# Kernel tuning notes

Hardware: AMD Instinct MI355X
Metric: run time of the kernel (lower is better)

The kernel has to match this reference:

```python
import jax, jax.numpy as jnp
import numpy as np


def _gru(x, w_ih, w_hh, b_ih, b_hh):
    # x: [B, T, D]; torch nn.GRU (batch_first) semantics, h0 = 0
    B = x.shape[0]
    H = w_hh.shape[1]
    def step(h, xt):
        gi = xt @ w_ih.T + b_ih          # [B, 3H]
        gh = h @ w_hh.T + b_hh           # [B, 3H]
        ir, iz, inn = jnp.split(gi, 3, axis=-1)
        hr, hz, hn = jnp.split(gh, 3, axis=-1)
        r = jax.nn.sigmoid(ir + hr)
        z = jax.nn.sigmoid(iz + hz)
        n = jnp.tanh(inn + r * hn)
        h_new = (1.0 - z) * n + z * h
        return h_new, h_new
    h0 = jnp.zeros((B, H), x.dtype)
    _, ys = jax.lax.scan(step, h0, jnp.swapaxes(x, 0, 1))
    return jnp.swapaxes(ys, 0, 1)        # [B, T, H]


def setup_inputs() -> dict:
    key = jax.random.key(0)
    ks = iter(jax.random.split(key, 40))
    def p(shape, scale=0.05):
        return jax.random.normal(next(ks), shape, dtype=jnp.float32) * scale
    B, T, Z, S = 1024, 2, 100, 6
    return {
        "x": p((B, T, Z, S), 1.0),
        # actor: GRU(6 -> 64) + SimpleSubActor(64 -> 512 -> 128 -> 1)
        "a_gru_wih": p((192, 6)), "a_gru_whh": p((192, 64)),
        "a_gru_bih": p((192,)), "a_gru_bhh": p((192,)),
        "a_fc1_w": p((512, 64)), "a_fc1_b": p((512,)),
        "a_fc2_w": p((128, 512)), "a_fc2_b": p((128,)),
        "a_fc3_w": p((1, 128)), "a_fc3_b": p((1,)),
        # critic: GRU(35 -> 32) + SimpleSubCritic(32 -> 512 -> 256 -> 1)
        "c_gru_wih": p((96, 35)), "c_gru_whh": p((96, 32)),
        "c_gru_bih": p((96,)), "c_gru_bhh": p((96,)),
        "c_fc1_w": p((512, 32)), "c_fc1_b": p((512,)),
        "c_fc2_w": p((256, 512)), "c_fc2_b": p((256,)),
        "c_fc3_w": p((1, 256)), "c_fc3_b": p((1,)),
        # LocalizedModule(35 -> 512 -> 256 -> 1)
        "lm_fc1_w": p((512, 35)), "lm_fc1_b": p((512,)),
        "lm_fc2_w": p((256, 512)), "lm_fc2_b": p((256,)),
        "lm_fc3_w": p((1, 256)), "lm_fc3_b": p((1,)),
    }


def reference(x, a_gru_wih, a_gru_whh, a_gru_bih, a_gru_bhh,
              a_fc1_w, a_fc1_b, a_fc2_w, a_fc2_b, a_fc3_w, a_fc3_b,
              c_gru_wih, c_gru_whh, c_gru_bih, c_gru_bhh,
              c_fc1_w, c_fc1_b, c_fc2_w, c_fc2_b, c_fc3_w, c_fc3_b,
              lm_fc1_w, lm_fc1_b, lm_fc2_w, lm_fc2_b, lm_fc3_w, lm_fc3_b):
    B, T, Z, S = x.shape
    # ---- SimpleActor: same GRU+MLP shared across zones -> batch zones ----
    # torch: a[i] from x[:, :, i]; torch.stack(a) -> [Z, B, T, 1], then .view(-1, T, Z)
    xz = jnp.transpose(x, (2, 0, 1, 3)).reshape(Z * B, T, S)   # zones-major
    sx = _gru(xz, a_gru_wih, a_gru_whh, a_gru_bih, a_gru_bhh)  # [Z*B, T, 64]
    h = jax.nn.relu(sx @ a_fc1_w.T + a_fc1_b)
    h = jax.nn.relu(h @ a_fc2_w.T + a_fc2_b)
    sa = h @ a_fc3_w.T + a_fc3_b                               # [Z*B, T, 1]
    p = sa.reshape(-1, T, Z)                                   # faithful view(-1, t, nzones)
    # ---- concat action onto state ----
    xc = jnp.concatenate([x, p.reshape(-1, T, Z, 1)], axis=-1)  # [B, T, Z, 7]
    # ---- SimpleCritic: f/q lists reset each iter -> only zone i=99 survives ----
    # neighbors of 99: (99, 89, 100->zeros, 109->zeros, 98)
    zeros = jnp.zeros_like(xc[:, :, Z - 1])
    xi = jnp.concatenate([xc[:, :, 99], xc[:, :, 89], zeros, zeros, xc[:, :, 98]], axis=2)  # [B, T, 35]
    # LocalizedModule on last timestep
    hf = jax.nn.relu(xi[:, -1, :] @ lm_fc1_w.T + lm_fc1_b)
    hf = jax.nn.relu(hf @ lm_fc2_w.T + lm_fc2_b)
    f = hf @ lm_fc3_w.T + lm_fc3_b                             # [B, 1]
    # critic GRU + SimpleSubCritic (it keeps only last timestep)
    xq = _gru(xi, c_gru_wih, c_gru_whh, c_gru_bih, c_gru_bhh)  # [B, T, 32]
    hq = jax.nn.relu(xq[:, -1, :] @ c_fc1_w.T + c_fc1_b)
    hq = jax.nn.relu(hq @ c_fc2_w.T + c_fc2_b)
    qz = hq @ c_fc3_w.T + c_fc3_b                              # [B, 1]
    q = jnp.sum(f + qz, axis=1)                                # [B]
    return p[:, -1], q.reshape(-1, 1)
```

## Files before the change

kernel.cpp:

```cpp
#include <hip/hip_runtime.h>
#include <hip/hip_bf16.h>

#define NB 1024
#define NT 2
#define NZ 100
#define NS 6
#define NSEQ (NZ*NB)

typedef short short8 __attribute__((ext_vector_type(8)));
typedef float floatx4 __attribute__((ext_vector_type(4)));
typedef unsigned int uint2v __attribute__((ext_vector_type(2)));

__device__ __forceinline__ float sigm(float v)     { return 1.0f/(1.0f + __expf(-v)); }
__device__ __forceinline__ float tanhfast(float v) { float t = __expf(2.0f*v); return 1.0f - 2.0f/(t + 1.0f); }
__device__ __forceinline__ unsigned short f2bf(float f) {
    __hip_bfloat16 h = __float2bfloat16(f);
    return *reinterpret_cast<unsigned short*>(&h);
}

#define WS_WIHB   819200
#define WS_WHHB   (WS_WIHB + 192*32*2)
#define WS_W1B    (WS_WHHB + 192*64*2)
#define WS_W2B    (WS_W1B + 512*64*2)
#define WS_L1WB   (WS_W2B + 128*512*2)
#define WS_L2WB   (WS_L1WB + 512*64*2)
#define WS_CF1WB  (WS_L2WB + 256*512*2)
#define WS_CF2WB  (WS_CF1WB + 512*32*2)
#define WS_CWIHB  (WS_CF2WB + 256*512*2)
#define WS_CWHHB  (WS_CWIHB + 96*64*2)

#define PREP_N (116736 + 32768 + 131072 + 16384 + 131072 + 6144 + 3072)

__global__ __launch_bounds__(256)
void prep_kernel(const float* __restrict__ wih, const float* __restrict__ whh,
                 const float* __restrict__ w1,  const float* __restrict__ w2,
                 const float* __restrict__ l1w, const float* __restrict__ l2w,
                 const float* __restrict__ cf1w, const float* __restrict__ cf2w,
                 const float* __restrict__ cwih, const float* __restrict__ cwhh,
                 unsigned short* wihb, unsigned short* whhb,
                 unsigned short* w1b,  unsigned short* w2b,
                 unsigned short* l1wb, unsigned short* l2wb,
                 unsigned short* cf1wb, unsigned short* cf2wb,
                 unsigned short* cwihb, unsigned short* cwhhb)
{
    int e = blockIdx.x*256 + threadIdx.x;
    if (e < 6144) {
        int g = e >> 5, k = e & 31;
        wihb[e] = f2bf(k < 6 ? wih[g*6 + k] : 0.0f);
    } else if (e < 18432) {
        int i = e - 6144;  whhb[i] = f2bf(whh[i]);
    } else if (e < 51200) {
        int i = e - 18432; w1b[i] = f2bf(w1[i]);
    } else if (e < 116736) {
        int i = e - 51200; w2b[i] = f2bf(w2[i]);
    } else if (e < 149504) {
        int i = e - 116736; int o = i >> 6, k = i & 63;
        l1wb[i] = f2bf(k < 35 ? l1w[o*35 + k] : 0.0f);
    } else if (e < 280576) {
        int i = e - 149504; l2wb[i] = f2bf(l2w[i]);
    } else if (e < 296960) {
        int i = e - 280576; cf1wb[i] = f2bf(cf1w[i]);
    } else if (e < 428032) {
        int i = e - 296960; cf2wb[i] = f2bf(cf2w[i]);
    } else if (e < 434176) {
        int i = e - 428032; int o = i >> 6, k = i & 63;
        cwihb[i] = f2bf(k < 35 ? cwih[o*35 + k] : 0.0f);
    } else if (e < PREP_N) {
        int i = e - 434176; cwhhb[i] = f2bf(cwhh[i]);
    }
}

__device__ __forceinline__ int swz(int r) { return (r & 7) << 4; }

__device__ __forceinline__ short8 ldsfrag(const char* base, int rowstride, int r, int k0) {
    int byte = r*rowstride + k0*2;
    byte ^= swz(r);
    return *reinterpret_cast<const short8*>(base + byte);
}

__device__ __forceinline__ short8 xfrag(const float* __restrict__ xp) {
    float2 a  = *reinterpret_cast<const float2*>(xp);
    float2 b2 = *reinterpret_cast<const float2*>(xp + 2);
    float2 c  = *reinterpret_cast<const float2*>(xp + 4);
    short8 f;
    f[0] = (short)f2bf(a.x);  f[1] = (short)f2bf(a.y);
    f[2] = (short)f2bf(b2.x); f[3] = (short)f2bf(b2.y);
    f[4] = (short)f2bf(c.x);  f[5] = (short)f2bf(c.y);
    f[6] = 0; f[7] = 0;
    return f;
}

__global__ __launch_bounds__(256)
void actor_mfma(const float* __restrict__ x,
                const unsigned short* __restrict__ wihb, const unsigned short* __restrict__ whhb,
                const float* __restrict__ bih, const float* __restrict__ bhh,
                const unsigned short* __restrict__ w1b, const float* __restrict__ b1,
                const unsigned short* __restrict__ w2b, const float* __restrict__ b2,
                const float* __restrict__ w3, const float* __restrict__ b3,
                float* __restrict__ sa, float* __restrict__ out0)
{
    __shared__ __align__(16) char smem[40960];
    char*  sxb  = smem;
    float* fc3p = (float*)smem;
    char*  h1b  = smem + 8192;

    const int tid  = threadIdx.x;
    const int wv   = tid >> 6;
    const int lane = tid & 63;
    const int r16  = lane & 15;
    const int g4   = lane >> 4;
    const int ft   = wv;
    const int s0   = blockIdx.x * 32;
    const int zz   = s0 >> 10;
    const int b0   = s0 & 1023;

    const int fb = ft*16 + g4*4;
    const floatx4 bihR = *reinterpret_cast<const floatx4*>(bih + fb);
    const floatx4 bihZ = *reinterpret_cast<const floatx4*>(bih + 64 + fb);
    const floatx4 bihN = *reinterpret_cast<const floatx4*>(bih + 128 + fb);
    const floatx4 bhhR = *reinterpret_cast<const floatx4*>(bhh + fb);
    const floatx4 bhhZ = *reinterpret_cast<const floatx4*>(bhh + 64 + fb);
    const floatx4 bhhN = *reinterpret_cast<const floatx4*>(bhh + 128 + fb);

    floatx4 h0v[2];
    floatx4 g1R[2], g1Z[2], g1N[2];

    {
        const short8 aR = *reinterpret_cast<const short8*>(wihb + ((ft     )*16 + r16)*32 + g4*8);
        const short8 aZ = *reinterpret_cast<const short8*>(wihb + ((ft +  4)*16 + r16)*32 + g4*8);
        const short8 aN = *reinterpret_cast<const short8*>(wihb + ((ft +  8)*16 + r16)*32 + g4*8);
        #pragma unroll
        for (int u = 0; u < 2; ++u) {
            const int seq = u*16 + r16;
            const float* xrow = x + (((b0 + seq)*NT)*NZ + zz)*NS;
            short8 bx0 = xfrag(xrow);
            short8 bx1 = xfrag(xrow + NZ*NS);
            floatx4 gR = {0,0,0,0}, gZ = {0,0,0,0}, gN = {0,0,0,0};
            gR = __builtin_amdgcn_mfma_f32_16x16x32_bf16(aR, bx0, gR, 0, 0, 0);
            gZ = __builtin_amdgcn_mfma_f32_16x16x32_bf16(aZ, bx0, gZ, 0, 0, 0);
            gN = __builtin_amdgcn_mfma_f32_16x16x32_bf16(aN, bx0, gN, 0, 0, 0);
            floatx4 tR = {0,0,0,0}, tZ = {0,0,0,0}, tN = {0,0,0,0};
            tR = __builtin_amdgcn_mfma_f32_16x16x32_bf16(aR, bx1, tR, 0, 0, 0);
            tZ = __builtin_amdgcn_mfma_f32_16x16x32_bf16(aZ, bx1, tZ, 0, 0, 0);
            tN = __builtin_amdgcn_mfma_f32_16x16x32_bf16(aN, bx1, tN, 0, 0, 0);
            g1R[u] = tR; g1Z[u] = tZ; g1N[u] = tN;
            floatx4 hh;
            #pragma unroll
            for (int q = 0; q < 4; ++q) {
                float r = sigm(gR[q] + bihR[q] + bhhR[q]);
                float z = sigm(gZ[q] + bihZ[q] + bhhZ[q]);
                float n = tanhfast(gN[q] + bihN[q] + r*bhhN[q]);
                hh[q] = (1.0f - z)*n;
            }
            h0v[u] = hh;
            unsigned int lo = (unsigned int)f2bf(hh[0]) | ((unsigned int)f2bf(hh[1]) << 16);
            unsigned int hi = (unsigned int)f2bf(hh[2]) | ((unsigned int)f2bf(hh[3]) << 16);
            uint2v vv = {lo, hi};
            int ba = seq*128 + fb*2; ba ^= swz(seq);
            *reinterpret_cast<uint2v*>(sxb + ba) = vv;
        }
    }
    __syncthreads();

    {
        const short8 wR0 = *reinterpret_cast<const short8*>(whhb + ((ft     )*16 + r16)*64 + g4*8);
        const short8 wR1 = *reinterpret_cast<const short8*>(whhb + ((ft     )*16 + r16)*64 + 32 + g4*8);
        const short8 wZ0 = *reinterpret_cast<const short8*>(whhb + ((ft +  4)*16 + r16)*64 + g4*8);
        const short8 wZ1 = *reinterpret_cast<const short8*>(whhb + ((ft +  4)*16 + r16)*64 + 32 + g4*8);
        const short8 wN0 = *reinterpret_cast<const short8*>(whhb + ((ft +  8)*16 + r16)*64 + g4*8);
        const short8 wN1 = *reinterpret_cast<const short8*>(whhb + ((ft +  8)*16 + r16)*64 + 32 + g4*8);
        #pragma unroll
        for (int u = 0; u < 2; ++u) {
            const int seq = u*16 + r16;
            short8 bh0 = ldsfrag(sxb, 128, seq, g4*8);
            short8 bh1 = ldsfrag(sxb, 128, seq, 32 + g4*8);
            floatx4 hR = {0,0,0,0}, hZ = {0,0,0,0}, hN = {0,0,0,0};
            hR = __builtin_amdgcn_mfma_f32_16x16x32_bf16(wR0, bh0, hR, 0, 0, 0);
            hZ = __builtin_amdgcn_mfma_f32_16x16x32_bf16(wZ0, bh0, hZ, 0, 0, 0);
            hN = __builtin_amdgcn_mfma_f32_16x16x32_bf16(wN0, bh0, hN, 0, 0, 0);
            hR = __builtin_amdgcn_mfma_f32_16x16x32_bf16(wR1, bh1, hR, 0, 0, 0);
            hZ = __builtin_amdgcn_mfma_f32_16x16x32_bf16(wZ1, bh1, hZ, 0, 0, 0);
            hN = __builtin_amdgcn_mfma_f32_16x16x32_bf16(wN1, bh1, hN, 0, 0, 0);
            floatx4 hn;
            #pragma unroll
            for (int q = 0; q < 4; ++q) {
                float r = sigm(g1R[u][q] + bihR[q] + hR[q] + bhhR[q]);
                float z = sigm(g1Z[u][q] + bihZ[q] + hZ[q] + bhhZ[q]);
                float n = tanhfast(g1N[u][q] + bihN[q] + r*(hN[q] + bhhN[q]));
                hn[q] = (1.0f - z)*n + z*h0v[u][q];
            }
            unsigned int lo = (unsigned int)f2bf(hn[0]) | ((unsigned int)f2bf(hn[1]) << 16);
            unsigned int hi = (unsigned int)f2bf(hn[2]) | ((unsigned int)f2bf(hn[3]) << 16);
            uint2v vv = {lo, hi};
            int row = 32 + seq;
            int ba = row*128 + fb*2; ba ^= swz(row);
            *reinterpret_cast<uint2v*>(sxb + ba) = vv;
        }
    }
    __syncthreads();

    short8 fr[4][2];
    #pragma unroll
    for (int rt = 0; rt < 4; ++rt) {
        fr[rt][0] = ldsfrag(sxb, 128, rt*16 + r16, g4*8);
        fr[rt][1] = ldsfrag(sxb, 128, rt*16 + r16, 32 + g4*8);
    }

    const int mt0 = wv*2, mt1 = wv*2 + 1;
    floatx4 acc[2][4];
    {
        const floatx4 bA = *reinterpret_cast<const floatx4*>(b2 + mt0*16 + g4*4);
        const floatx4 bB = *reinterpret_cast<const floatx4*>(b2 + mt1*16 + g4*4);
        #pragma unroll
        for (int rt = 0; rt < 4; ++rt) { acc[0][rt] = bA; acc[1][rt] = bB; }
    }

    #pragma unroll
    for (int h = 0; h < 2; ++h) {
        #pragma unroll
        for (int j = 0; j < 4; ++j) {
            int mtg = h*16 + wv*4 + j;
            int mtl = wv*4 + j;
            const short8 a0 = *reinterpret_cast<const short8*>(w1b + (mtg*16 + r16)*64 + g4*8);
            const short8 a1 = *reinterpret_cast<const short8*>(w1b + (mtg*16 + r16)*64 + 32 + g4*8);
            const floatx4 bias = *reinterpret_cast<const floatx4*>(b1 + mtg*16 + g4*4);
            #pragma unroll
            for (int rt = 0; rt < 4; ++rt) {
                floatx4 a = bias;
                a = __builtin_amdgcn_mfma_f32_16x16x32_bf16(a0, fr[rt][0], a, 0, 0, 0);
                a = __builtin_amdgcn_mfma_f32_16x16x32_bf16(a1, fr[rt][1], a, 0, 0, 0);
                unsigned int lo = (unsigned int)f2bf(fmaxf(a[0],0.f)) | ((unsigned int)f2bf(fmaxf(a[1],0.f)) << 16);
                unsigned int hi = (unsigned int)f2bf(fmaxf(a[2],0.f)) | ((unsigned int)f2bf(fmaxf(a[3],0.f)) << 16);
                int row = rt*16 + r16;
                int byte = row*512 + (mtl*16 + g4*4)*2; byte ^= swz(row);
                uint2v vv = {lo, hi};
                *reinterpret_cast<uint2v*>(h1b + byte) = vv;
            }
        }
        __syncthreads();

        {
            const unsigned short* wp0 = w2b + (mt0*16 + r16)*512 + h*256 + g4*8;
            const unsigned short* wp1 = w2b + (mt1*16 + r16)*512 + h*256 + g4*8;
            #pragma unroll
            for (int ks = 0; ks < 8; ++ks) {
                const short8 a0 = *reinterpret_cast<const short8*>(wp0 + ks*32);
                const short8 a1 = *reinterpret_cast<const short8*>(wp1 + ks*32);
                #pragma unroll
                for (int rt = 0; rt < 4; ++rt) {
                    short8 bb = ldsfrag(h1b, 512, rt*16 + r16, ks*32 + g4*8);
                    acc[0][rt] = __builtin_amdgcn_mfma_f32_16x16x32_bf16(a0, bb, acc[0][rt], 0, 0, 0);
                    acc[1][rt] = __builtin_amdgcn_mfma_f32_16x16x32_bf16(a1, bb, acc[1][rt], 0, 0, 0);
                }
            }
        }
        if (h == 0) __syncthreads();
    }

    {
        const floatx4 w3a = *reinterpret_cast<const floatx4*>(w3 + mt0*16 + g4*4);
        const floatx4 w3b = *reinterpret_cast<const floatx4*>(w3 + mt1*16 + g4*4);
        #pragma unroll
        for (int rt = 0; rt < 4; ++rt) {
            float p = fmaxf(acc[0][rt][0],0.f)*w3a[0] + fmaxf(acc[0][rt][1],0.f)*w3a[1]
                    + fmaxf(acc[0][rt][2],0.f)*w3a[2] + fmaxf(acc[0][rt][3],0.f)*w3a[3]
                    + fmaxf(acc[1][rt][0],0.f)*w3b[0] + fmaxf(acc[1][rt][1],0.f)*w3b[1]
                    + fmaxf(acc[1][rt][2],0.f)*w3b[2] + fmaxf(acc[1][rt][3],0.f)*w3b[3];
            p += __shfl_xor(p, 16);
            p += __shfl_xor(p, 32);
            if (g4 == 0) fc3p[wv*64 + rt*16 + r16] = p;
        }
    }
    __syncthreads();

    if (tid < 64) {
        float v = b3[0];
        #pragma unroll
        for (int w = 0; w < 4; ++w) v += fc3p[w*64 + tid];
        int t = tid >> 5, sl = tid & 31;
        int gseq = s0 + sl;
        int i = gseq*2 + t;
        sa[i] = v;
        int m = i % 200;
        if (m >= 100) out0[(i/200)*NZ + (m - 100)] = v;
    }
}

__global__ __launch_bounds__(512)
void critic_mfma(const float* __restrict__ x, const float* __restrict__ sa,
                 const unsigned short* __restrict__ cwihb, const unsigned short* __restrict__ cwhhb,
                 const float* __restrict__ cbih, const float* __restrict__ cbhh,
                 const unsigned short* __restrict__ cf1wb, const float* __restrict__ cf1b,
                 const unsigned short* __restrict__ cf2wb, const float* __restrict__ cf2b,
                 const float* __restrict__ cf3w, const float* __restrict__ cf3b,
                 const unsigned short* __restrict__ l1wb, const float* __restrict__ l1b,
                 const unsigned short* __restrict__ l2wb, const float* __restrict__ l2b,
                 const float* __restrict__ l3w, const float* __restrict__ l3b,
                 float* __restrict__ outq)
{
    __shared__ __align__(16) char smem[25600];
    char*  xib = smem;
    char*  h1b = smem + 4096;
    char*  h0b = smem + 20480;
    char*  hqb = smem + 22528;
    float* fp  = (float*)(smem + 24576);
    float* qp  = (float*)(smem + 25088);

    const int tid  = threadIdx.x;
    const int wv   = tid >> 6;
    const int lane = tid & 63;
    const int r16  = lane & 15;
    const int g4   = lane >> 4;
    const int b0   = blockIdx.x * 16;

    for (int e = tid; e < 2048; e += 512) {
        int trow = e >> 6, k = e & 63;
        int t = trow >> 4, row = trow & 15;
        int b = b0 + row;
        float v = 0.0f;
        if (k < 35) {
            int slot = k / 7, s = k - slot*7;
            int nb = (slot==0)?99:((slot==1)?89:((slot==4)?98:-1));
            if (nb >= 0) v = (s < 6) ? x[((b*NT + t)*NZ + nb)*NS + s]
                                     : sa[b*200 + t*100 + nb];
        }
        int byte = trow*128 + k*2; byte ^= ((trow & 7) << 4);
        *reinterpret_cast<unsigned short*>(xib + byte) = f2bf(v);
    }
    __syncthreads();

    {
        short8 bx0 = ldsfrag(xib, 128, 16 + r16, g4*8);
        short8 bx1 = ldsfrag(xib, 128, 16 + r16, 32 + g4*8);
        #pragma unroll
        for (int j = 0; j < 4; ++j) {
            int mt = wv*4 + j;
            const short8 a0 = *reinterpret_cast<const short8*>(l1wb + (mt*16 + r16)*64 + g4*8);
            const short8 a1 = *reinterpret_cast<const short8*>(l1wb + (mt*16 + r16)*64 + 32 + g4*8);
            floatx4 acc = *reinterpret_cast<const floatx4*>(l1b + mt*16 + g4*4);
            acc = __builtin_amdgcn_mfma_f32_16x16x32_bf16(a0, bx0, acc, 0, 0, 0);
            acc = __builtin_amdgcn_mfma_f32_16x16x32_bf16(a1, bx1, acc, 0, 0, 0);
            unsigned int lo = (unsigned int)f2bf(fmaxf(acc[0],0.f)) | ((unsigned int)f2bf(fmaxf(acc[1],0.f)) << 16);
            unsigned int hi = (unsigned int)f2bf(fmaxf(acc[2],0.f)) | ((unsigned int)f2bf(fmaxf(acc[3],0.f)) << 16);
            int byte = r16*1024 + (mt*16 + g4*4)*2; byte ^= ((r16 & 7) << 4);
            uint2v vv = {lo, hi};
            *reinterpret_cast<uint2v*>(h1b + byte) = vv;
        }
    }
    __syncthreads();

    {
        int mt0 = wv*2, mt1 = wv*2 + 1;
        floatx4 acc0 = *reinterpret_cast<const floatx4*>(l2b + mt0*16 + g4*4);
        floatx4 acc1 = *reinterpret_cast<const floatx4*>(l2b + mt1*16 + g4*4);
        const unsigned short* wp0 = l2wb + (mt0*16 + r16)*512 + g4*8;
        const unsigned short* wp1 = l2wb + (mt1*16 + r16)*512 + g4*8;
        for (int ks = 0; ks < 16; ++ks) {
            short8 bb = ldsfrag(h1b, 1024, r16, ks*32 + g4*8);
            const short8 a0 = *reinterpret_cast<const short8*>(wp0 + ks*32);
            const short8 a1 = *reinterpret_cast<const short8*>(wp1 + ks*32);
            acc0 = __builtin_amdgcn_mfma_f32_16x16x32_bf16(a0, bb, acc0, 0, 0, 0);
            acc1 = __builtin_amdgcn_mfma_f32_16x16x32_bf16(a1, bb, acc1, 0, 0, 0);
        }
        const floatx4 w0 = *reinterpret_cast<const floatx4*>(l3w + mt0*16 + g4*4);
        const floatx4 w1 = *reinterpret_cast<const floatx4*>(l3w + mt1*16 + g4*4);
        float p = fmaxf(acc0[0],0.f)*w0[0] + fmaxf(acc0[1],0.f)*w0[1]
                + fmaxf(acc0[2],0.f)*w0[2] + fmaxf(acc0[3],0.f)*w0[3]
                + fmaxf(acc1[0],0.f)*w1[0] + fmaxf(acc1[1],0.f)*w1[1]
                + fmaxf(acc1[2],0.f)*w1[2] + fmaxf(acc1[3],0.f)*w1[3];
        p += __shfl_xor(p, 16);
        p += __shfl_xor(p, 32);
        if (g4 == 0) fp[wv*16 + r16] = p;
    }
    __syncthreads();

    floatx4 h0r = {0,0,0,0};
    floatx4 gR1 = {0,0,0,0}, gZ1 = {0,0,0,0}, gN1 = {0,0,0,0};
    floatx4 bihR, bihZ, bihN, bhhR, bhhZ, bhhN;
    if (wv < 2) {
        const int hf = wv;
        const int fb = hf*16 + g4*4;
        bihR = *reinterpret_cast<const floatx4*>(cbih + fb);
        bihZ = *reinterpret_cast<const floatx4*>(cbih + 32 + fb);
        bihN = *reinterpret_cast<const floatx4*>(cbih + 64 + fb);
        bhhR = *reinterpret_cast<const floatx4*>(cbhh + fb);
        bhhZ = *reinterpret_cast<const floatx4*>(cbhh + 32 + fb);
        bhhN = *reinterpret_cast<const floatx4*>(cbhh + 64 + fb);
        short8 bx0 = ldsfrag(xib, 128, r16, g4*8);
        short8 bx1 = ldsfrag(xib, 128, r16, 32 + g4*8);
        short8 cx0 = ldsfrag(xib, 128, 16 + r16, g4*8);
        short8 cx1 = ldsfrag(xib, 128, 16 + r16, 32 + g4*8);
        floatx4 gR0 = {0,0,0,0}, gZ0 = {0,0,0,0}, gN0 = {0,0,0,0};
        #pragma unroll
        for (int p = 0; p < 2; ++p) {
            const short8 aR = *reinterpret_cast<const short8*>(cwihb + ((hf    )*16 + r16)*64 + p*32 + g4*8);
            const short8 aZ = *reinterpret_cast<const short8*>(cwihb + ((2+hf  )*16 + r16)*64 + p*32 + g4*8);
            const short8 aN = *reinterpret_cast<const short8*>(cwihb + ((4+hf  )*16 + r16)*64 + p*32 + g4*8);
            short8 b0f = p ? bx1 : bx0;
            short8 b1f = p ? cx1 : cx0;
            gR0 = __builtin_amdgcn_mfma_f32_16x16x32_bf16(aR, b0f, gR0, 0, 0, 0);
            gZ0 = __builtin_amdgcn_mfma_f32_16x16x32_bf16(aZ, b0f, gZ0, 0, 0, 0);
            gN0 = __builtin_amdgcn_mfma_f32_16x16x32_bf16(aN, b0f, gN0, 0, 0, 0);
            gR1 = __builtin_amdgcn_mfma_f32_16x16x32_bf16(aR, b1f, gR1, 0, 0, 0);
            gZ1 = __builtin_amdgcn_mfma_f32_16x16x32_bf16(aZ, b1f, gZ1, 0, 0, 0);
            gN1 = __builtin_amdgcn_mfma_f32_16x16x32_bf16(aN, b1f, gN1, 0, 0, 0);
        }
        #pragma unroll
        for (int q = 0; q < 4; ++q) {
            float r = sigm(gR0[q] + bihR[q] + bhhR[q]);
            float z = sigm(gZ0[q] + bihZ[q] + bhhZ[q]);
            float n = tanhfast(gN0[q] + bihN[q] + r*bhhN[q]);
            h0r[q] = (1.0f - z)*n;
        }
        unsigned int lo = (unsigned int)f2bf(h0r[0]) | ((unsigned int)f2bf(h0r[1]) << 16);
        unsigned int hi = (unsigned int)f2bf(h0r[2]) | ((unsigned int)f2bf(h0r[3]) << 16);
        uint2v vv = {lo, hi};
        int byte = r16*128 + fb*2; byte ^= ((r16 & 7) << 4);
        *reinterpret_cast<uint2v*>(h0b + byte) = vv;
    }
    __syncthreads();
    if (wv < 2) {
        const int hf = wv;
        const int fb = hf*16 + g4*4;
        short8 bh = ldsfrag(h0b, 128, r16, g4*8);
        const short8 aR = *reinterpret_cast<const short8*>(cwhhb + ((hf    )*16 + r16)*32 + g4*8);
        const short8 aZ = *reinterpret_cast<const short8*>(cwhhb + ((2+hf  )*16 + r16)*32 + g4*8);
        const short8 aN = *reinterpret_cast<const short8*>(cwhhb + ((4+hf  )*16 + r16)*32 + g4*8);
        floatx4 hR = {0,0,0,0}, hZ = {0,0,0,0}, hN = {0,0,0,0};
        hR = __builtin_amdgcn_mfma_f32_16x16x32_bf16(aR, bh, hR, 0, 0, 0);
        hZ = __builtin_amdgcn_mfma_f32_16x16x32_bf16(aZ, bh, hZ, 0, 0, 0);
        hN = __builtin_amdgcn_mfma_f32_16x16x32_bf16(aN, bh, hN, 0, 0, 0);
        floatx4 hn;
        #pragma unroll
        for (int q = 0; q < 4; ++q) {
            float r = sigm(gR1[q] + bihR[q] + hR[q] + bhhR[q]);
            float z = sigm(gZ1[q] + bihZ[q] + hZ[q] + bhhZ[q]);
            float n = tanhfast(gN1[q] + bihN[q] + r*(hN[q] + bhhN[q]));
            hn[q] = (1.0f - z)*n + z*h0r[q];
        }
        unsigned int lo = (unsigned int)f2bf(hn[0]) | ((unsigned int)f2bf(hn[1]) << 16);
        unsigned int hi = (unsigned int)f2bf(hn[2]) | ((unsigned int)f2bf(hn[3]) << 16);
        uint2v vv = {lo, hi};
        int byte = r16*128 + fb*2; byte ^= ((r16 & 7) << 4);
        *reinterpret_cast<uint2v*>(hqb + byte) = vv;
    }
    __syncthreads();

    {
        short8 bq = ldsfrag(hqb, 128, r16, g4*8);
        #pragma unroll
        for (int j = 0; j < 4; ++j) {
            int mt = wv*4 + j;
            const short8 a = *reinterpret_cast<const short8*>(cf1wb + (mt*16 + r16)*32 + g4*8);
            floatx4 acc = *reinterpret_cast<const floatx4*>(cf1b + mt*16 + g4*4);
            acc = __builtin_amdgcn_mfma_f32_16x16x32_bf16(a, bq, acc, 0, 0, 0);
            unsigned int lo = (unsigned int)f2bf(fmaxf(acc[0],0.f)) | ((unsigned int)f2bf(fmaxf(acc[1],0.f)) << 16);
            unsigned int hi = (unsigned int)f2bf(fmaxf(acc[2],0.f)) | ((unsigned int)f2bf(fmaxf(acc[3],0.f)) << 16);
            int byte = r16*1024 + (mt*16 + g4*4)*2; byte ^= ((r16 & 7) << 4);
            uint2v vv = {lo, hi};
            *reinterpret_cast<uint2v*>(h1b + byte) = vv;
        }
    }
    __syncthreads();

    {
        int mt0 = wv*2, mt1 = wv*2 + 1;
        floatx4 acc0 = *reinterpret_cast<const floatx4*>(cf2b + mt0*16 + g4*4);
        floatx4 acc1 = *reinterpret_cast<const floatx4*>(cf2b + mt1*16 + g4*4);
        const unsigned short* wp0 = cf2wb + (mt0*16 + r16)*512 + g4*8;
        const unsigned short* wp1 = cf2wb + (mt1*16 + r16)*512 + g4*8;
        for (int ks = 0; ks < 16; ++ks) {
            short8 bb = ldsfrag(h1b, 1024, r16, ks*32 + g4*8);
            const short8 a0 = *reinterpret_cast<const short8*>(wp0 + ks*32);
            const short8 a1 = *reinterpret_cast<const short8*>(wp1 + ks*32);
            acc0 = __builtin_amdgcn_mfma_f32_16x16x32_bf16(a0, bb, acc0, 0, 0, 0);
            acc1 = __builtin_amdgcn_mfma_f32_16x16x32_bf16(a1, bb, acc1, 0, 0, 0);
        }
        const floatx4 w0 = *reinterpret_cast<const floatx4*>(cf3w + mt0*16 + g4*4);
        const floatx4 w1 = *reinterpret_cast<const floatx4*>(cf3w + mt1*16 + g4*4);
        float p = fmaxf(acc0[0],0.f)*w0[0] + fmaxf(acc0[1],0.f)*w0[1]
                + fmaxf(acc0[2],0.f)*w0[2] + fmaxf(acc0[3],0.f)*w0[3]
                + fmaxf(acc1[0],0.f)*w1[0] + fmaxf(acc1[1],0.f)*w1[1]
                + fmaxf(acc1[2],0.f)*w1[2] + fmaxf(acc1[3],0.f)*w1[3];
        p += __shfl_xor(p, 16);
        p += __shfl_xor(p, 32);
        if (g4 == 0) qp[wv*16 + r16] = p;
    }
    __syncthreads();

    if (tid < 16) {
        float f = l3b[0], qz = cf3b[0];
        #pragma unroll
        for (int w = 0; w < 8; ++w) { f += fp[w*16 + tid]; qz += qp[w*16 + tid]; }
        outq[b0 + tid] = f + qz;
    }
}

extern "C" void kernel_launch(void* const* d_in, const int* in_sizes, int n_in,
                              void* d_out, int out_size, void* d_ws, size_t ws_size,
                              hipStream_t stream)
{
    (void)in_sizes; (void)n_in; (void)out_size; (void)ws_size;
    const float* x     = (const float*)d_in[0];
    const float* a_wih = (const float*)d_in[1];
    const float* a_whh = (const float*)d_in[2];
    const float* a_bih = (const float*)d_in[3];
    const float* a_bhh = (const float*)d_in[4];
    const float* a1w   = (const float*)d_in[5];
    const float* a1b   = (const float*)d_in[6];
    const float* a2w   = (const float*)d_in[7];
    const float* a2b   = (const float*)d_in[8];
    const float* a3w   = (const float*)d_in[9];
    const float* a3b   = (const float*)d_in[10];
    const float* cwih  = (const float*)d_in[11];
    const float* cwhh  = (const float*)d_in[12];
    const float* cbih  = (const float*)d_in[13];
    const float* cbhh  = (const float*)d_in[14];
    const float* cf1w  = (const float*)d_in[15];
    const float* cf1b  = (const float*)d_in[16];
    const float* cf2w  = (const float*)d_in[17];
    const float* cf2b  = (const float*)d_in[18];
    const float* cf3w  = (const float*)d_in[19];
    const float* cf3b  = (const float*)d_in[20];
    const float* l1w   = (const float*)d_in[21];
    const float* l1b   = (const float*)d_in[22];
    const float* l2w   = (const float*)d_in[23];
    const float* l2b   = (const float*)d_in[24];
    const float* l3w   = (const float*)d_in[25];
    const float* l3b   = (const float*)d_in[26];

    float* sa = (float*)d_ws;
    unsigned short* wihb  = (unsigned short*)((char*)d_ws + WS_WIHB);
    unsigned short* whhb  = (unsigned short*)((char*)d_ws + WS_WHHB);
    unsigned short* w1b   = (unsigned short*)((char*)d_ws + WS_W1B);
    unsigned short* w2b   = (unsigned short*)((char*)d_ws + WS_W2B);
    unsigned short* l1wb  = (unsigned short*)((char*)d_ws + WS_L1WB);
    unsigned short* l2wb  = (unsigned short*)((char*)d_ws + WS_L2WB);
    unsigned short* cf1wb = (unsigned short*)((char*)d_ws + WS_CF1WB);
    unsigned short* cf2wb = (unsigned short*)((char*)d_ws + WS_CF2WB);
    unsigned short* cwihb = (unsigned short*)((char*)d_ws + WS_CWIHB);
    unsigned short* cwhhb = (unsigned short*)((char*)d_ws + WS_CWHHB);
    float* out0 = (float*)d_out;
    float* outq = (float*)d_out + NB*NZ;

    hipLaunchKernelGGL(prep_kernel, dim3((PREP_N + 255)/256), dim3(256), 0, stream,
                       a_wih, a_whh, a1w, a2w, l1w, l2w, cf1w, cf2w, cwih, cwhh,
                       wihb, whhb, w1b, w2b, l1wb, l2wb, cf1wb, cf2wb, cwihb, cwhhb);
    hipLaunchKernelGGL(actor_mfma, dim3(NSEQ/32), dim3(256), 0, stream,
                       x, wihb, whhb, a_bih, a_bhh, w1b, a1b, w2b, a2b, a3w, a3b, sa, out0);
    hipLaunchKernelGGL(critic_mfma, dim3(NB/16), dim3(512), 0, stream,
                       x, sa, cwihb, cwhhb, cbih, cbhh, cf1wb, cf1b, cf2wb, cf2b, cf3w, cf3b,
                       l1wb, l1b, l2wb, l2b, l3w, l3b, outq);
}
```

Before: 131.9 us.

## Double-buffer fc1/fc2 in quarter chunks to overlap actor MLP stages

Splits the actor's fc1 hidden dimension into four 128-wide quarters stored in two alternating LDS buffers. Each fc2 chunk now runs alongside the fc1 computation of the next quarter, which removes one barrier-separated serial phase per half and gives the scheduler independent MFMA work to interleave. The cost is more barriers (four instead of three) and a different LDS row stride, which depends on the swizzle staying conflict-free at 256-byte rows.

```diff
diff --git a/kernel.cpp b/kernel.cpp
--- a/kernel.cpp
+++ b/kernel.cpp
@@ -102,7 +102,8 @@
     __shared__ __align__(16) char smem[40960];
     char*  sxb  = smem;
     float* fc3p = (float*)smem;
-    char*  h1b  = smem + 8192;
+    char*  q0b  = smem + 8192;
+    char*  q1b  = smem + 24576;
 
     const int tid  = threadIdx.x;
     const int wv   = tid >> 6;
@@ -214,13 +215,14 @@
         #pragma unroll
         for (int rt = 0; rt < 4; ++rt) { acc[0][rt] = bA; acc[1][rt] = bB; }
     }
-
-    #pragma unroll
-    for (int h = 0; h < 2; ++h) {
-        #pragma unroll
-        for (int j = 0; j < 4; ++j) {
-            int mtg = h*16 + wv*4 + j;
-            int mtl = wv*4 + j;
+    const unsigned short* wp0base = w2b + (mt0*16 + r16)*512 + g4*8;
+    const unsigned short* wp1base = w2b + (mt1*16 + r16)*512 + g4*8;
+
+    auto FC1Q = [&](int q, char* buf) {
+        #pragma unroll
+        for (int j = 0; j < 2; ++j) {
+            int mtg = q*8 + wv*2 + j;
+            int mtl = wv*2 + j;
             const short8 a0 = *reinterpret_cast<const short8*>(w1b + (mtg*16 + r16)*64 + g4*8);
             const short8 a1 = *reinterpret_cast<const short8*>(w1b + (mtg*16 + r16)*64 + 32 + g4*8);
             const floatx4 bias = *reinterpret_cast<const floatx4*>(b1 + mtg*16 + g4*4);
@@ -232,30 +234,37 @@
                 unsigned int lo = (unsigned int)f2bf(fmaxf(a[0],0.f)) | ((unsigned int)f2bf(fmaxf(a[1],0.f)) << 16);
                 unsigned int hi = (unsigned int)f2bf(fmaxf(a[2],0.f)) | ((unsigned int)f2bf(fmaxf(a[3],0.f)) << 16);
                 int row = rt*16 + r16;
-                int byte = row*512 + (mtl*16 + g4*4)*2; byte ^= swz(row);
+                int byte = row*256 + (mtl*16 + g4*4)*2; byte ^= swz(row);
                 uint2v vv = {lo, hi};
-                *reinterpret_cast<uint2v*>(h1b + byte) = vv;
+                *reinterpret_cast<uint2v*>(buf + byte) = vv;
             }
         }
-        __syncthreads();
-
-        {
-            const unsigned short* wp0 = w2b + (mt0*16 + r16)*512 + h*256 + g4*8;
-            const unsigned short* wp1 = w2b + (mt1*16 + r16)*512 + h*256 + g4*8;
+    };
+    auto FC2Q = [&](int q, const char* buf) {
+        const unsigned short* wp0 = wp0base + q*128;
+        const unsigned short* wp1 = wp1base + q*128;
+        #pragma unroll
+        for (int ks = 0; ks < 4; ++ks) {
+            const short8 a0 = *reinterpret_cast<const short8*>(wp0 + ks*32);
+            const short8 a1 = *reinterpret_cast<const short8*>(wp1 + ks*32);
             #pragma unroll
-            for (int ks = 0; ks < 8; ++ks) {
-                const short8 a0 = *reinterpret_cast<const short8*>(wp0 + ks*32);
-                const short8 a1 = *reinterpret_cast<const short8*>(wp1 + ks*32);
-                #pragma unroll
-                for (int rt = 0; rt < 4; ++rt) {
-                    short8 bb = ldsfrag(h1b, 512, rt*16 + r16, ks*32 + g4*8);
-                    acc[0][rt] = __builtin_amdgcn_mfma_f32_16x16x32_bf16(a0, bb, acc[0][rt], 0, 0, 0);
-                    acc[1][rt] = __builtin_amdgcn_mfma_f32_16x16x32_bf16(a1, bb, acc[1][rt], 0, 0, 0);
-                }
+            for (int rt = 0; rt < 4; ++rt) {
+                short8 bb = ldsfrag(buf, 256, rt*16 + r16, ks*32 + g4*8);
+                acc[0][rt] = __builtin_amdgcn_mfma_f32_16x16x32_bf16(a0, bb, acc[0][rt], 0, 0, 0);
+                acc[1][rt] = __builtin_amdgcn_mfma_f32_16x16x32_bf16(a1, bb, acc[1][rt], 0, 0, 0);
             }
         }
-        if (h == 0) __syncthreads();
-    }
+    };
+
+    FC1Q(0, q0b);
+    __syncthreads();
+    FC2Q(0, q0b); FC1Q(1, q1b);
+    __syncthreads();
+    FC2Q(1, q1b); FC1Q(2, q0b);
+    __syncthreads();
+    FC2Q(2, q0b); FC1Q(3, q1b);
+    __syncthreads();
+    FC2Q(3, q1b);
 
     {
         const floatx4 w3a = *reinterpret_cast<const floatx4*>(w3 + mt0*16 + g4*4);
```

Measured after the change: 135.7 us. 2.9% more time.
